# Optimization experiments

Hardware: AMD Instinct MI355X
Metric: run time of the kernel (lower is better)

Reference implementation:

```python
import jax, jax.numpy as jnp
import numpy as np

B, C, H, W = 8, 3, 1024, 1024


def setup_inputs() -> dict:
    key = jax.random.key(0)
    k1, k2, k3, k4, k5, k6 = jax.random.split(key, 6)
    return {
        "diagAtA": jax.random.uniform(k1, (B, C, H, W), dtype=jnp.float32),
        "Aty": jax.random.normal(k2, (B, C, H, W), dtype=jnp.float32),
        "mk": jax.random.normal(k3, (B, C, H, W), dtype=jnp.float32),
        "lambdak": jax.random.uniform(k4, (B, C, H, W), dtype=jnp.float32),
        "gamma_n": jax.random.uniform(k5, (1,), dtype=jnp.float32),
        "gamma_p": jax.random.uniform(k6, (1,), dtype=jnp.float32),
        "scale": 2,
    }


def reference(diagAtA, Aty, mk, lambdak, gamma_n, gamma_p, scale):
    roll = jnp.roll
    # diag(D^T diag(lambda) D) for horizontal and vertical differences
    diagDhtlambdakDh = lambdak + roll(lambdak, -1, axis=3)
    diagDvtlambdakDv = lambdak + roll(lambdak, -1, axis=2)
    diagDtlambdakD = diagDhtlambdakDh + diagDvtlambdakDv

    invSigma_r = jax.nn.relu(gamma_n * diagAtA + gamma_p * diagDtlambdakD) + 0.0001

    # A = decimation by `scale`, A^T = zero-insertion upsampling (SurDirect1/SurTranspose1)
    Amk = mk[:, :, ::scale, ::scale]
    AtAmk = jnp.zeros_like(mk).at[:, :, ::scale, ::scale].set(Amk)

    Dh = lambda x: x - roll(x, 1, axis=3)
    Dv = lambda x: x - roll(x, 1, axis=2)
    Dht = lambda x: x - roll(x, -1, axis=3)
    Dvt = lambda x: x - roll(x, -1, axis=2)

    m_r = (
        gamma_n * (Aty - AtAmk + diagAtA * mk)
        - gamma_p * (Dht(lambdak * Dh(mk)) + Dvt(lambdak * Dv(mk)))
        + gamma_p * diagDtlambdakD * mk
    ) / invSigma_r
    return (m_r, invSigma_r)
```

## Files before the change

kernel.cpp:

```cpp
#include <hip/hip_runtime.h>


#define HH 1024
#define WW 1024
#define NPLANES 24
#define VECS_PER_ROW (WW/4)

__global__ __launch_bounds__(256) void rmodule_kernel(
    const float* __restrict__ diagAtA,
    const float* __restrict__ Aty,
    const float* __restrict__ mk,
    const float* __restrict__ lambdak,
    const float* __restrict__ gamma_n_p,
    const float* __restrict__ gamma_p_p,
    const int*   __restrict__ scale_p,
    float* __restrict__ out_m_r,
    float* __restrict__ out_invSigma)
{
    const int idx = blockIdx.x * blockDim.x + threadIdx.x;
    const int total_vec = NPLANES * HH * VECS_PER_ROW;
    if (idx >= total_vec) return;

    const float gn = gamma_n_p[0];
    const float gp = gamma_p_p[0];
    const int scale = scale_p[0];

    const int row   = idx >> 8;
    const int w0    = (idx & 255) << 2;
    const int h     = row & (HH - 1);
    const int plane = row >> 10;

    const int base = plane * HH * WW;
    const int rowC = base + h * WW;
    const int hU = (h == 0)      ? HH - 1 : h - 1;
    const int hD = (h == HH - 1) ? 0      : h + 1;
    const int rowU = base + hU * WW;
    const int rowD = base + hD * WW;

    const float4 lam  = *reinterpret_cast<const float4*>(lambdak + rowC + w0);
    const float4 lamD = *reinterpret_cast<const float4*>(lambdak + rowD + w0);
    const float4 m    = *reinterpret_cast<const float4*>(mk      + rowC + w0);
    const float4 mU   = *reinterpret_cast<const float4*>(mk      + rowU + w0);
    const float4 mD   = *reinterpret_cast<const float4*>(mk      + rowD + w0);
    const float4 a    = *reinterpret_cast<const float4*>(diagAtA + rowC + w0);
    const float4 ay   = *reinterpret_cast<const float4*>(Aty     + rowC + w0);

    const int wR = (w0 + 4) & (WW - 1);
    const int wL = (w0 - 1) & (WW - 1);
    const float lam_r4 = lambdak[rowC + wR];
    const float m_r4   = mk[rowC + wR];
    const float m_lm1  = mk[rowC + wL];

    const float lamv[5]  = {lam.x, lam.y, lam.z, lam.w, lam_r4};
    const float mv[6]    = {m_lm1, m.x, m.y, m.z, m.w, m_r4};
    const float lamDv[4] = {lamD.x, lamD.y, lamD.z, lamD.w};
    const float mUv[4]   = {mU.x, mU.y, mU.z, mU.w};
    const float mDv[4]   = {mD.x, mD.y, mD.z, mD.w};
    const float av[4]    = {a.x, a.y, a.z, a.w};
    const float ayv[4]   = {ay.x, ay.y, ay.z, ay.w};

    const bool hOnGrid = (h % scale) == 0;
    int rw = w0 % scale;

    float outm[4], outs[4];
#pragma unroll
    for (int i = 0; i < 4; ++i) {
        const float lam_c = lamv[i];
        const float lam_e = lamv[i + 1];
        const float lam_s = lamDv[i];
        const float m_c   = mv[i + 1];
        const float m_w   = mv[i];
        const float m_e   = mv[i + 2];
        const float m_n   = mUv[i];
        const float m_s   = mDv[i];

        const float diagD = 2.0f * lam_c + lam_e + lam_s;
        const float is = fmaxf(gn * av[i] + gp * diagD, 0.0f) + 0.0001f;

        const float atamk = (hOnGrid && (rw == 0)) ? m_c : 0.0f;
        rw++; if (rw == scale) rw = 0;

        const float dh = lam_c * (m_c - m_w) - lam_e * (m_e - m_c);
        const float dv = lam_c * (m_c - m_n) - lam_s * (m_s - m_c);

        const float num = gn * (ayv[i] - atamk + av[i] * m_c)
                        - gp * (dh + dv)
                        + gp * diagD * m_c;
        outm[i] = num / is;
        outs[i] = is;
    }

    *reinterpret_cast<float4*>(out_m_r     + rowC + w0) =
        make_float4(outm[0], outm[1], outm[2], outm[3]);
    *reinterpret_cast<float4*>(out_invSigma + rowC + w0) =
        make_float4(outs[0], outs[1], outs[2], outs[3]);
}

extern "C" void kernel_launch(void* const* d_in, const int* in_sizes, int n_in,
                              void* d_out, int out_size, void* d_ws, size_t ws_size,
                              hipStream_t stream) {
    const float* diagAtA = (const float*)d_in[0];
    const float* Aty     = (const float*)d_in[1];
    const float* mk      = (const float*)d_in[2];
    const float* lambdak = (const float*)d_in[3];
    const float* gamma_n = (const float*)d_in[4];
    const float* gamma_p = (const float*)d_in[5];
    const int*   scale   = (const int*)d_in[6];

    float* out = (float*)d_out;
    const int n = out_size / 2;
    float* out_m_r      = out;
    float* out_invSigma = out + n;

    const int total_vec = NPLANES * HH * VECS_PER_ROW;
    const int block = 256;
    const int grid = (total_vec + block - 1) / block;
    rmodule_kernel<<<grid, block, 0, stream>>>(
        diagAtA, Aty, mk, lambdak, gamma_n, gamma_p, scale,
        out_m_r, out_invSigma);
}
```

Before: 454.9 us.

## Process two rows by eight columns per thread with nontemporal streaming and XCD block swizzle

Each thread now computes a 2x8 output tile, so the vertically adjacent mk and lambdak rows are shared in registers instead of being reloaded by neighbouring threads. Streaming-only inputs and both outputs use nontemporal loads and stores to reduce cache pollution. Block indices are permuted so that each XCD works on a contiguous region. In exchange, register pressure rises and fewer threads are in flight.

```diff
diff --git a/kernel.cpp b/kernel.cpp
--- a/kernel.cpp
+++ b/kernel.cpp
@@ -3,8 +3,14 @@
 
 #define HH 1024
 #define WW 1024
-#define NPLANES 24
-#define VECS_PER_ROW (WW/4)
+#define NP 24
+#define NBLOCKS (NP * HH / 4)
+
+typedef float f4 __attribute__((ext_vector_type(4)));
+
+#define FILL8(dst, va, vb) \
+    { (dst)[0]=(va).x; (dst)[1]=(va).y; (dst)[2]=(va).z; (dst)[3]=(va).w; \
+      (dst)[4]=(vb).x; (dst)[5]=(vb).y; (dst)[6]=(vb).z; (dst)[7]=(vb).w; }
 
 __global__ __launch_bounds__(256) void rmodule_kernel(
     const float* __restrict__ diagAtA,
@@ -17,83 +23,135 @@
     float* __restrict__ out_m_r,
     float* __restrict__ out_invSigma)
 {
-    const int idx = blockIdx.x * blockDim.x + threadIdx.x;
-    const int total_vec = NPLANES * HH * VECS_PER_ROW;
-    if (idx >= total_vec) return;
+    const int b  = blockIdx.x;
+    const int lb = (b & 7) * (NBLOCKS / 8) + (b >> 3);
+
+    const int t    = threadIdx.x;
+    const int rp   = lb * 2 + (t >> 7);
+    const int lane = t & 127;
+    const int w0   = lane << 3;
+
+    const int plane = rp >> 9;
+    const int h0  = (rp & 511) << 1;
+    const int h1  = h0 + 1;
+    const int hm1 = (h0 == 0)      ? (HH - 1) : (h0 - 1);
+    const int h2  = (h1 == HH - 1) ? 0        : (h1 + 1);
+
+    const int base = plane * (HH * WW);
+    const float* __restrict__ mkp = mk + base;
+    const float* __restrict__ lmp = lambdak + base;
+
+    const int rm1 = hm1 * WW, r0 = h0 * WW, r1 = h1 * WW, r2 = h2 * WW;
 
     const float gn = gamma_n_p[0];
     const float gp = gamma_p_p[0];
     const int scale = scale_p[0];
 
-    const int row   = idx >> 8;
-    const int w0    = (idx & 255) << 2;
-    const int h     = row & (HH - 1);
-    const int plane = row >> 10;
+    #define LD4(p)  (*reinterpret_cast<const f4*>(p))
+    #define LDNT(p) (__builtin_nontemporal_load(reinterpret_cast<const f4*>(p)))
+    #define STNT(v, p) __builtin_nontemporal_store((v), reinterpret_cast<f4*>(p))
 
-    const int base = plane * HH * WW;
-    const int rowC = base + h * WW;
-    const int hU = (h == 0)      ? HH - 1 : h - 1;
-    const int hD = (h == HH - 1) ? 0      : h + 1;
-    const int rowU = base + hU * WW;
-    const int rowD = base + hD * WW;
+    const f4 Mm1a = LD4(mkp + rm1 + w0), Mm1b = LD4(mkp + rm1 + w0 + 4);
+    const f4 M0a  = LD4(mkp + r0  + w0), M0b  = LD4(mkp + r0  + w0 + 4);
+    const f4 M1a  = LD4(mkp + r1  + w0), M1b  = LD4(mkp + r1  + w0 + 4);
+    const f4 M2a  = LD4(mkp + r2  + w0), M2b  = LD4(mkp + r2  + w0 + 4);
+    const f4 L0a  = LD4(lmp + r0  + w0), L0b  = LD4(lmp + r0  + w0 + 4);
+    const f4 L1a  = LD4(lmp + r1  + w0), L1b  = LD4(lmp + r1  + w0 + 4);
+    const f4 L2a  = LD4(lmp + r2  + w0), L2b  = LD4(lmp + r2  + w0 + 4);
+    const f4 A0a = LDNT(diagAtA + base + r0 + w0);
+    const f4 A0b = LDNT(diagAtA + base + r0 + w0 + 4);
+    const f4 A1a = LDNT(diagAtA + base + r1 + w0);
+    const f4 A1b = LDNT(diagAtA + base + r1 + w0 + 4);
+    const f4 Y0a = LDNT(Aty     + base + r0 + w0);
+    const f4 Y0b = LDNT(Aty     + base + r0 + w0 + 4);
+    const f4 Y1a = LDNT(Aty     + base + r1 + w0);
+    const f4 Y1b = LDNT(Aty     + base + r1 + w0 + 4);
 
-    const float4 lam  = *reinterpret_cast<const float4*>(lambdak + rowC + w0);
-    const float4 lamD = *reinterpret_cast<const float4*>(lambdak + rowD + w0);
-    const float4 m    = *reinterpret_cast<const float4*>(mk      + rowC + w0);
-    const float4 mU   = *reinterpret_cast<const float4*>(mk      + rowU + w0);
-    const float4 mD   = *reinterpret_cast<const float4*>(mk      + rowD + w0);
-    const float4 a    = *reinterpret_cast<const float4*>(diagAtA + rowC + w0);
-    const float4 ay   = *reinterpret_cast<const float4*>(Aty     + rowC + w0);
+    const int wR = (w0 + 8) & (WW - 1);
+    const int wL = (w0 - 1) & (WW - 1);
+    const float m0l = mkp[r0 + wL], m0r = mkp[r0 + wR];
+    const float m1l = mkp[r1 + wL], m1r = mkp[r1 + wR];
+    const float l0r = lmp[r0 + wR], l1r = lmp[r1 + wR];
 
-    const int wR = (w0 + 4) & (WW - 1);
-    const int wL = (w0 - 1) & (WW - 1);
-    const float lam_r4 = lambdak[rowC + wR];
-    const float m_r4   = mk[rowC + wR];
-    const float m_lm1  = mk[rowC + wL];
+    const int rw_init = w0 % scale;
 
-    const float lamv[5]  = {lam.x, lam.y, lam.z, lam.w, lam_r4};
-    const float mv[6]    = {m_lm1, m.x, m.y, m.z, m.w, m_r4};
-    const float lamDv[4] = {lamD.x, lamD.y, lamD.z, lamD.w};
-    const float mUv[4]   = {mU.x, mU.y, mU.z, mU.w};
-    const float mDv[4]   = {mD.x, mD.y, mD.z, mD.w};
-    const float av[4]    = {a.x, a.y, a.z, a.w};
-    const float ayv[4]   = {ay.x, ay.y, ay.z, ay.w};
+    {
+        float lamR[9]; FILL8(lamR, L0a, L0b); lamR[8] = l0r;
+        float lamS[8]; FILL8(lamS, L1a, L1b);
+        float mC[10];  mC[0] = m0l; FILL8((mC + 1), M0a, M0b); mC[9] = m0r;
+        float mN[8];   FILL8(mN, Mm1a, Mm1b);
+        float mS[8];   FILL8(mS, M1a, M1b);
+        float av[8];   FILL8(av, A0a, A0b);
+        float yv[8];   FILL8(yv, Y0a, Y0b);
 
-    const bool hOnGrid = (h % scale) == 0;
-    int rw = w0 % scale;
-
-    float outm[4], outs[4];
+        const bool hOn = (h0 % scale) == 0;
+        int rw = rw_init;
+        float om[8], os[8];
 #pragma unroll
-    for (int i = 0; i < 4; ++i) {
-        const float lam_c = lamv[i];
-        const float lam_e = lamv[i + 1];
-        const float lam_s = lamDv[i];
-        const float m_c   = mv[i + 1];
-        const float m_w   = mv[i];
-        const float m_e   = mv[i + 2];
-        const float m_n   = mUv[i];
-        const float m_s   = mDv[i];
-
-        const float diagD = 2.0f * lam_c + lam_e + lam_s;
-        const float is = fmaxf(gn * av[i] + gp * diagD, 0.0f) + 0.0001f;
-
-        const float atamk = (hOnGrid && (rw == 0)) ? m_c : 0.0f;
-        rw++; if (rw == scale) rw = 0;
-
-        const float dh = lam_c * (m_c - m_w) - lam_e * (m_e - m_c);
-        const float dv = lam_c * (m_c - m_n) - lam_s * (m_s - m_c);
-
-        const float num = gn * (ayv[i] - atamk + av[i] * m_c)
-                        - gp * (dh + dv)
-                        + gp * diagD * m_c;
-        outm[i] = num / is;
-        outs[i] = is;
+        for (int i = 0; i < 8; ++i) {
+            const float lam_c = lamR[i], lam_e = lamR[i + 1], lam_s = lamS[i];
+            const float m_c = mC[i + 1], m_w = mC[i], m_e = mC[i + 2];
+            const float m_n = mN[i], m_s = mS[i];
+            const float diagD = 2.0f * lam_c + lam_e + lam_s;
+            const float is = fmaxf(gn * av[i] + gp * diagD, 0.0f) + 0.0001f;
+            const float atamk = (hOn && rw == 0) ? m_c : 0.0f;
+            rw++; if (rw == scale) rw = 0;
+            const float dh = lam_c * (m_c - m_w) - lam_e * (m_e - m_c);
+            const float dv = lam_c * (m_c - m_n) - lam_s * (m_s - m_c);
+            const float num = gn * (yv[i] - atamk + av[i] * m_c)
+                            - gp * (dh + dv) + gp * diagD * m_c;
+            om[i] = num / is;
+            os[i] = is;
+        }
+        f4 v;
+        v.x = om[0]; v.y = om[1]; v.z = om[2]; v.w = om[3];
+        STNT(v, out_m_r + base + r0 + w0);
+        v.x = om[4]; v.y = om[5]; v.z = om[6]; v.w = om[7];
+        STNT(v, out_m_r + base + r0 + w0 + 4);
+        v.x = os[0]; v.y = os[1]; v.z = os[2]; v.w = os[3];
+        STNT(v, out_invSigma + base + r0 + w0);
+        v.x = os[4]; v.y = os[5]; v.z = os[6]; v.w = os[7];
+        STNT(v, out_invSigma + base + r0 + w0 + 4);
     }
 
-    *reinterpret_cast<float4*>(out_m_r     + rowC + w0) =
-        make_float4(outm[0], outm[1], outm[2], outm[3]);
-    *reinterpret_cast<float4*>(out_invSigma + rowC + w0) =
-        make_float4(outs[0], outs[1], outs[2], outs[3]);
+    {
+        float lamR[9]; FILL8(lamR, L1a, L1b); lamR[8] = l1r;
+        float lamS[8]; FILL8(lamS, L2a, L2b);
+        float mC[10];  mC[0] = m1l; FILL8((mC + 1), M1a, M1b); mC[9] = m1r;
+        float mN[8];   FILL8(mN, M0a, M0b);
+        float mS[8];   FILL8(mS, M2a, M2b);
+        float av[8];   FILL8(av, A1a, A1b);
+        float yv[8];   FILL8(yv, Y1a, Y1b);
+
+        const bool hOn = (h1 % scale) == 0;
+        int rw = rw_init;
+        float om[8], os[8];
+#pragma unroll
+        for (int i = 0; i < 8; ++i) {
+            const float lam_c = lamR[i], lam_e = lamR[i + 1], lam_s = lamS[i];
+            const float m_c = mC[i + 1], m_w = mC[i], m_e = mC[i + 2];
+            const float m_n = mN[i], m_s = mS[i];
+            const float diagD = 2.0f * lam_c + lam_e + lam_s;
+            const float is = fmaxf(gn * av[i] + gp * diagD, 0.0f) + 0.0001f;
+            const float atamk = (hOn && rw == 0) ? m_c : 0.0f;
+            rw++; if (rw == scale) rw = 0;
+            const float dh = lam_c * (m_c - m_w) - lam_e * (m_e - m_c);
+            const float dv = lam_c * (m_c - m_n) - lam_s * (m_s - m_c);
+            const float num = gn * (yv[i] - atamk + av[i] * m_c)
+                            - gp * (dh + dv) + gp * diagD * m_c;
+            om[i] = num / is;
+            os[i] = is;
+        }
+        f4 v;
+        v.x = om[0]; v.y = om[1]; v.z = om[2]; v.w = om[3];
+        STNT(v, out_m_r + base + r1 + w0);
+        v.x = om[4]; v.y = om[5]; v.z = om[6]; v.w = om[7];
+        STNT(v, out_m_r + base + r1 + w0 + 4);
+        v.x = os[0]; v.y = os[1]; v.z = os[2]; v.w = os[3];
+        STNT(v, out_invSigma + base + r1 + w0);
+        v.x = os[4]; v.y = os[5]; v.z = os[6]; v.w = os[7];
+        STNT(v, out_invSigma + base + r1 + w0 + 4);
+    }
 }
 
 extern "C" void kernel_launch(void* const* d_in, const int* in_sizes, int n_in,
@@ -109,13 +167,7 @@
 
     float* out = (float*)d_out;
     const int n = out_size / 2;
-    float* out_m_r      = out;
-    float* out_invSigma = out + n;
-
-    const int total_vec = NPLANES * HH * VECS_PER_ROW;
-    const int block = 256;
-    const int grid = (total_vec + block - 1) / block;
-    rmodule_kernel<<<grid, block, 0, stream>>>(
+    rmodule_kernel<<<NBLOCKS, 256, 0, stream>>>(
         diagAtA, Aty, mk, lambdak, gamma_n, gamma_p, scale,
-        out_m_r, out_invSigma);
+        out, out + n);
 }
```

New measurement: 556.8 us. 22.4% more time.
